# Optimization experiments

Measured on AMD Instinct MI355X. Metric: run time of the kernel, lower is better.

The kernel has to match this reference:

```python
import jax, jax.numpy as jnp
import numpy as np

N = 6            # ensemble members (must match share_mode '6-1')
IN_C = 128
OUT_C = 128
K = 3
STRIDE = 1
PAD = 1
D = IN_C * OUT_C * K * K  # 147456
TEMP = 1.0
ZP1 = 1.2
ZP2 = -0.2
RES_DENOS = (3.0, 5.0)   # res_denos[:maxBWPow] with bw=2 -> [2**2-1, 2**2+1]


def round_ste(v):
    # straight-through round: forward round, backward identity
    return v + jax.lax.stop_gradient(jnp.round(v) - v)


def setup_inputs() -> dict:
    key = jax.random.key(0)
    k1, k2, k3, k4 = jax.random.split(key, 4)
    x = jax.random.normal(k1, (48, IN_C, 64, 64), jnp.float32)
    U = jax.random.normal(k2, (N, D), jnp.float32)
    bp = jax.random.normal(k3, (N + 1, D), jnp.float32)
    # uniform noise for the gumbel-sigmoid sample (open interval to avoid log(0))
    u = jax.random.uniform(k4, (N + 1, D), jnp.float32, 1e-6, 1.0 - 1e-6)
    return {"x": x, "U": U, "bp": bp, "u": u}


def reference(x, U, bp, u):
    beta = jnp.max(U)
    alpha = jnp.min(U)

    # gumbel-sigmoid gating
    g = jnp.log(u / (1.0 - u))
    bsamples = jax.nn.sigmoid((g + bp) / TEMP)
    gates = jnp.clip(bsamples * (ZP1 - ZP2) + ZP2, 0.0, 1.0)  # (7, D)
    # first 6 rows: per-member gates for level 0; last row shared across members for level 1
    gates = jnp.stack([gates[:N], jnp.broadcast_to(gates[N:], (N, D))], axis=0)  # (2, N, D)
    order_gates = jax.lax.stop_gradient(
        jnp.cumprod((gates > 0).astype(gates.dtype), axis=0)
    )

    # sequential residual-bit STE quantization (2 levels)
    s1 = (beta - alpha) / RES_DENOS[0]
    v1 = s1 * round_ste(U / s1)                       # (N, D)
    s2 = s1 / RES_DENOS[1]
    v2 = s2 * round_ste((U - v1.mean(0)) / s2)        # (N, D); vals.sum(0).mean(0) == v1.mean(0)
    vals = jnp.stack([v1, v2], axis=0)                # (2, N, D)

    w = (vals * (gates * order_gates)).sum(0)         # (N, D)
    w = w.reshape(OUT_C * N, IN_C, K, K)

    B = x.shape[0]
    xr = x.reshape(B // N, N * x.shape[1], x.shape[2], x.shape[3])
    act = jax.lax.conv_general_dilated(
        xr, w,
        window_strides=(STRIDE, STRIDE),
        padding=[(PAD, PAD), (PAD, PAD)],
        dimension_numbers=('NCHW', 'OIHW', 'NCHW'),
        feature_group_count=N,
    )
    return act.reshape(act.shape[0] * N, act.shape[1] // N, act.shape[2], act.shape[3])
```

## Files before the change

### kernel.cpp

```cpp
#include <hip/hip_runtime.h>
#include <stdint.h>

typedef __attribute__((ext_vector_type(8))) short bf16x8;
typedef __attribute__((ext_vector_type(4))) float f32x4;

#define DW 147456
#define NTOT (6 * DW)

__device__ __forceinline__ unsigned short f2bf(float f) {
    unsigned int u = __float_as_uint(f);
    u = (u + 0x7FFFu + ((u >> 16) & 1u)) >> 16;
    return (unsigned short)u;
}

__global__ __launch_bounds__(256) void reduce_part(const float* __restrict__ U,
                                                   float* __restrict__ part) {
    int tid = threadIdx.x;
    float mx = -INFINITY, mn = INFINITY;
    for (int i = blockIdx.x * 256 + tid; i < NTOT; i += 256 * 256) {
        float v = U[i];
        mx = fmaxf(mx, v);
        mn = fminf(mn, v);
    }
    __shared__ float smx[256], smn[256];
    smx[tid] = mx; smn[tid] = mn;
    __syncthreads();
    for (int s = 128; s > 0; s >>= 1) {
        if (tid < s) {
            smx[tid] = fmaxf(smx[tid], smx[tid + s]);
            smn[tid] = fminf(smn[tid], smn[tid + s]);
        }
        __syncthreads();
    }
    if (tid == 0) { part[blockIdx.x] = smx[0]; part[256 + blockIdx.x] = smn[0]; }
}

__global__ __launch_bounds__(256) void reduce_final(const float* __restrict__ part,
                                                    float* __restrict__ scal) {
    int tid = threadIdx.x;
    __shared__ float smx[256], smn[256];
    smx[tid] = part[tid]; smn[tid] = part[256 + tid];
    __syncthreads();
    for (int s = 128; s > 0; s >>= 1) {
        if (tid < s) {
            smx[tid] = fmaxf(smx[tid], smx[tid + s]);
            smn[tid] = fminf(smn[tid], smn[tid + s]);
        }
        __syncthreads();
    }
    if (tid == 0) { scal[0] = smx[0]; scal[1] = smn[0]; }
}

__global__ __launch_bounds__(256) void make_weights(const float* __restrict__ U,
                                                    const float* __restrict__ bp,
                                                    const float* __restrict__ uu,
                                                    const float* __restrict__ scal,
                                                    unsigned short* __restrict__ Wb2) {
    int d = blockIdx.x * 256 + threadIdx.x;
    if (d >= DW) return;
    float beta = scal[0], alpha = scal[1];
    float s1 = (beta - alpha) / 3.0f;
    float s2 = s1 / 5.0f;

    float v1[6]; float vsum = 0.f;
    #pragma unroll
    for (int n = 0; n < 6; n++) {
        float Un = U[n * DW + d];
        float v = s1 * rintf(Un / s1);
        v1[n] = v; vsum += v;
    }
    float vmean = vsum / 6.0f;

    float g6;
    {
        float un = uu[6 * DW + d];
        float g = logf(un / (1.0f - un));
        float sg = 1.0f / (1.0f + expf(-(g + bp[6 * DW + d])));
        g6 = fminf(fmaxf(sg * 1.4f - 0.2f, 0.0f), 1.0f);
    }

    int oc = d / 1152;
    int rem = d - oc * 1152;
    int ic = rem / 9;
    int t9 = rem - ic * 9;
    int c = ic >> 5, icc = ic & 31;
    size_t base = ((size_t)c * 9 + t9) * 4096 + (size_t)oc * 32 + icc;

    #pragma unroll
    for (int n = 0; n < 6; n++) {
        float un = uu[n * DW + d];
        float g = logf(un / (1.0f - un));
        float sg = 1.0f / (1.0f + expf(-(g + bp[n * DW + d])));
        float g0 = fminf(fmaxf(sg * 1.4f - 0.2f, 0.0f), 1.0f);
        float Un = U[n * DW + d];
        float v2 = s2 * rintf((Un - vmean) / s2);
        float w = v1[n] * g0 + ((g0 > 0.0f && g6 > 0.0f) ? v2 * g6 : 0.0f);
        Wb2[(size_t)n * DW + base] = f2bf(w);
    }
}

__global__ __launch_bounds__(256) void transform_x(const float* __restrict__ x,
                                                   unsigned short* __restrict__ xT) {
    __shared__ unsigned short Sh[128 * 70];
    int b = blockIdx.x;
    int img = b >> 6, row = b & 63;
    int tid = threadIdx.x;
    {
        int ch = tid >> 1;
        int col0 = (tid & 1) * 32;
        const float* src = x + (((size_t)(img * 128 + ch) * 64 + row) * 64 + col0);
        #pragma unroll
        for (int j = 0; j < 8; j++) {
            float4 v = ((const float4*)src)[j];
            unsigned int p0 = (unsigned int)f2bf(v.x) | ((unsigned int)f2bf(v.y) << 16);
            unsigned int p1 = (unsigned int)f2bf(v.z) | ((unsigned int)f2bf(v.w) << 16);
            unsigned int* dst = (unsigned int*)&Sh[ch * 70 + col0 + j * 4];
            dst[0] = p0; dst[1] = p1;
        }
    }
    __syncthreads();
    {
        int col = tid & 63;
        int chg = (tid >> 6) * 32;
        union { unsigned short s[32]; uint4 v[4]; } tmp;
        #pragma unroll
        for (int j = 0; j < 32; j++) tmp.s[j] = Sh[(chg + j) * 70 + col];
        uint4* dst = (uint4*)(xT + (((size_t)(img * 64 + row) * 64 + col) * 128 + chg));
        #pragma unroll
        for (int k = 0; k < 4; k++) dst[k] = tmp.v[k];
    }
}

__global__ __launch_bounds__(256) void conv_mfma(const unsigned short* __restrict__ xT,
                                                 const unsigned short* __restrict__ Wb2,
                                                 float* __restrict__ out) {
    __shared__ __align__(16) unsigned short Xs[4096];
    __shared__ __align__(16) unsigned short Ws[4096];
    int blk = blockIdx.x;
    int img = blk >> 5;
    int row0 = (blk & 31) * 2;
    int mem = img - (img / 6) * 6;
    const unsigned short* Wsrc = Wb2 + (size_t)mem * DW;
    const unsigned short* Xsrc = xT + (size_t)img * 524288;

    int tid = threadIdx.x;
    int lane = tid & 63;
    int wave = tid >> 6;
    int ocbase = (wave & 1) * 64;
    int pxbase = (wave >> 1) * 64;
    int lr = lane & 15, lq = lane >> 4;

    f32x4 acc[4][4];
    #pragma unroll
    for (int mi = 0; mi < 4; mi++)
        #pragma unroll
        for (int ni = 0; ni < 4; ni++)
            acc[mi][ni] = (f32x4){0.f, 0.f, 0.f, 0.f};

    for (int c = 0; c < 4; c++) {
        for (int t = 0; t < 9; t++) {
            int dy = t / 3;
            int dx = t - dy * 3;
            #pragma unroll
            for (int ii = 0; ii < 2; ii++) {
                int i = tid + ii * 256;
                int px = i >> 2, cc = i & 3;
                int srow = row0 + (px >> 6) + dy - 1;
                int scol = (px & 63) + dx - 1;
                uint4 v = make_uint4(0u, 0u, 0u, 0u);
                if ((unsigned)srow < 64u && (unsigned)scol < 64u)
                    v = *(const uint4*)(Xsrc + ((srow * 64 + scol) * 128 + c * 32 + cc * 8));
                *(uint4*)(Xs + i * 8) = v;
            }
            const unsigned short* wp = Wsrc + (c * 9 + t) * 4096;
            #pragma unroll
            for (int ii = 0; ii < 2; ii++) {
                int i = tid + ii * 256;
                *(uint4*)(Ws + i * 8) = *(const uint4*)(wp + i * 8);
            }
            __syncthreads();
            bf16x8 af[4], bfr[4];
            #pragma unroll
            for (int mi = 0; mi < 4; mi++)
                af[mi] = *(const bf16x8*)(Ws + (ocbase + mi * 16 + lr) * 32 + lq * 8);
            #pragma unroll
            for (int ni = 0; ni < 4; ni++)
                bfr[ni] = *(const bf16x8*)(Xs + (pxbase + ni * 16 + lr) * 32 + lq * 8);
            #pragma unroll
            for (int mi = 0; mi < 4; mi++)
                #pragma unroll
                for (int ni = 0; ni < 4; ni++)
                    acc[mi][ni] = __builtin_amdgcn_mfma_f32_16x16x32_bf16(
                        af[mi], bfr[ni], acc[mi][ni], 0, 0, 0);
            __syncthreads();
        }
    }
    float* obase = out + (size_t)img * 524288 + row0 * 64;
    #pragma unroll
    for (int mi = 0; mi < 4; mi++) {
        #pragma unroll
        for (int ni = 0; ni < 4; ni++) {
            int px = pxbase + ni * 16 + lr;
            int ocb = ocbase + mi * 16 + lq * 4;
            #pragma unroll
            for (int rr = 0; rr < 4; rr++)
                obase[(size_t)(ocb + rr) * 4096 + px] = acc[mi][ni][rr];
        }
    }
}

extern "C" void kernel_launch(void* const* d_in, const int* in_sizes, int n_in,
                              void* d_out, int out_size, void* d_ws, size_t ws_size,
                              hipStream_t stream) {
    const float* x  = (const float*)d_in[0];
    const float* U  = (const float*)d_in[1];
    const float* bp = (const float*)d_in[2];
    const float* uu = (const float*)d_in[3];
    float* out = (float*)d_out;

    char* ws = (char*)d_ws;
    float* part = (float*)ws;
    float* scal = (float*)(ws + 2048);
    unsigned short* Wb2 = (unsigned short*)(ws + 4096);
    unsigned short* xT  = (unsigned short*)(ws + 4096 + 1769472);

    reduce_part <<<256, 256, 0, stream>>>(U, part);
    reduce_final<<<1, 256, 0, stream>>>(part, scal);
    make_weights<<<576, 256, 0, stream>>>(U, bp, uu, scal, Wb2);
    transform_x <<<48 * 64, 256, 0, stream>>>(x, xT);
    conv_mfma   <<<48 * 32, 256, 0, stream>>>(xT, Wb2, out);
}
```

Baseline: 313.6 us.

## Stage halo input tile once per channel chunk and double-buffer weights via LDS DMA

The conv kernel now loads a 4-row by 66-column haloed input tile into LDS once per 32-channel chunk. All nine taps read it at shifted offsets, replacing a separate global gather per tap. Weight tiles are prefetched one iteration ahead into a double buffer with global_load_lds, so global-memory latency can overlap the MFMA work. The cost is more LDS use, an extra barrier at each chunk boundary, and full unrolling of the loop, which may raise code size and register pressure.

Result: faster. 277.7 us (-11.5%).

```diff
diff --git a/kernel.cpp b/kernel.cpp
--- a/kernel.cpp
+++ b/kernel.cpp
@@ -131,11 +131,14 @@
     }
 }
 
+typedef const __attribute__((address_space(1))) void CGV;
+typedef __attribute__((address_space(3))) void LV;
+
 __global__ __launch_bounds__(256) void conv_mfma(const unsigned short* __restrict__ xT,
                                                  const unsigned short* __restrict__ Wb2,
                                                  float* __restrict__ out) {
-    __shared__ __align__(16) unsigned short Xs[4096];
-    __shared__ __align__(16) unsigned short Ws[4096];
+    __shared__ __align__(16) unsigned short Xs[4 * 66 * 32];
+    __shared__ __align__(16) unsigned short Wd[2][4096];
     int blk = blockIdx.x;
     int img = blk >> 5;
     int row0 = (blk & 31) * 2;
@@ -147,7 +150,7 @@
     int lane = tid & 63;
     int wave = tid >> 6;
     int ocbase = (wave & 1) * 64;
-    int pxbase = (wave >> 1) * 64;
+    int prow = wave >> 1;
     int lr = lane & 15, lq = lane >> 4;
 
     f32x4 acc[4][4];
@@ -157,35 +160,55 @@
         for (int ni = 0; ni < 4; ni++)
             acc[mi][ni] = (f32x4){0.f, 0.f, 0.f, 0.f};
 
+    auto prefetchW = [&](int it, int buf) {
+        const unsigned short* wp = Wsrc + it * 4096;
+        #pragma unroll
+        for (int k = 0; k < 2; k++) {
+            __builtin_amdgcn_global_load_lds((CGV*)(wp + (tid + k * 256) * 8),
+                                             (LV*)(&Wd[buf][(tid + k * 256) * 8]),
+                                             16, 0, 0);
+        }
+    };
+
+    auto stageX = [&](int c) {
+        #pragma unroll
+        for (int k = 0; k < 3; k++) {
+            int i = tid + k * 256;
+            if (i < 528) {
+                int r = i / 132;
+                int rem = i - r * 132;
+                int cl = rem >> 1, half = rem & 1;
+                int srow = row0 + r - 1;
+                int scol = cl - 1;
+                uint4 v0 = make_uint4(0u, 0u, 0u, 0u), v1 = v0;
+                if ((unsigned)srow < 64u && (unsigned)scol < 64u) {
+                    const uint4* p = (const uint4*)(Xsrc + ((srow * 64 + scol) * 128 + c * 32 + half * 16));
+                    v0 = p[0]; v1 = p[1];
+                }
+                uint4* d = (uint4*)(Xs + i * 16);
+                d[0] = v0; d[1] = v1;
+            }
+        }
+    };
+
+    prefetchW(0, 0);
+    stageX(0);
+    __syncthreads();
+
+    #pragma unroll
     for (int c = 0; c < 4; c++) {
+        #pragma unroll
         for (int t = 0; t < 9; t++) {
-            int dy = t / 3;
-            int dx = t - dy * 3;
-            #pragma unroll
-            for (int ii = 0; ii < 2; ii++) {
-                int i = tid + ii * 256;
-                int px = i >> 2, cc = i & 3;
-                int srow = row0 + (px >> 6) + dy - 1;
-                int scol = (px & 63) + dx - 1;
-                uint4 v = make_uint4(0u, 0u, 0u, 0u);
-                if ((unsigned)srow < 64u && (unsigned)scol < 64u)
-                    v = *(const uint4*)(Xsrc + ((srow * 64 + scol) * 128 + c * 32 + cc * 8));
-                *(uint4*)(Xs + i * 8) = v;
-            }
-            const unsigned short* wp = Wsrc + (c * 9 + t) * 4096;
-            #pragma unroll
-            for (int ii = 0; ii < 2; ii++) {
-                int i = tid + ii * 256;
-                *(uint4*)(Ws + i * 8) = *(const uint4*)(wp + i * 8);
-            }
-            __syncthreads();
+            int it = c * 9 + t;
+            if (it + 1 < 36) prefetchW(it + 1, (it + 1) & 1);
+            int dy = t / 3, dx = t - dy * 3;
             bf16x8 af[4], bfr[4];
             #pragma unroll
             for (int mi = 0; mi < 4; mi++)
-                af[mi] = *(const bf16x8*)(Ws + (ocbase + mi * 16 + lr) * 32 + lq * 8);
+                af[mi] = *(const bf16x8*)(&Wd[it & 1][(ocbase + mi * 16 + lr) * 32 + lq * 8]);
             #pragma unroll
             for (int ni = 0; ni < 4; ni++)
-                bfr[ni] = *(const bf16x8*)(Xs + (pxbase + ni * 16 + lr) * 32 + lq * 8);
+                bfr[ni] = *(const bf16x8*)(Xs + (((prow + dy) * 66 + ni * 16 + lr + dx) * 32 + lq * 8));
             #pragma unroll
             for (int mi = 0; mi < 4; mi++)
                 #pragma unroll
@@ -193,14 +216,16 @@
                     acc[mi][ni] = __builtin_amdgcn_mfma_f32_16x16x32_bf16(
                         af[mi], bfr[ni], acc[mi][ni], 0, 0, 0);
             __syncthreads();
-        }
-    }
+            if (t == 8 && c < 3) { stageX(c + 1); __syncthreads(); }
+        }
+    }
+
     float* obase = out + (size_t)img * 524288 + row0 * 64;
     #pragma unroll
     for (int mi = 0; mi < 4; mi++) {
         #pragma unroll
         for (int ni = 0; ni < 4; ni++) {
-            int px = pxbase + ni * 16 + lr;
+            int px = prow * 64 + ni * 16 + lr;
             int ocb = ocbase + mi * 16 + lq * 4;
             #pragma unroll
             for (int rr = 0; rr < 4; rr++)
```
